# Performance work log

Hardware: AMD Instinct MI355X
Metric: run time of the kernel (lower is better)

## Reference

```python
import jax, jax.numpy as jnp
import numpy as np

N_NODES = 50000
N_EDGES = 800000
IN_F = 128
HID = 32
HEADS = 8
N_CLASSES = 40
OUT_HEADS = 1
NEG_SLOPE = 0.2


def _glorot(key, shape):
    fan_in, fan_out = shape[0], int(np.prod(shape[1:]))
    s = jnp.sqrt(6.0 / (fan_in + fan_out))
    return jax.random.uniform(key, shape, jnp.float32, -s, s)


def setup_inputs() -> dict:
    key = jax.random.key(0)
    ks = jax.random.split(key, 12)
    x = jax.random.normal(ks[0], (N_NODES, IN_F), jnp.float32)
    src = jax.random.randint(ks[1], (N_EDGES,), 0, N_NODES, jnp.int32)
    dst = jax.random.randint(ks[2], (N_EDGES,), 0, N_NODES, jnp.int32)
    # layer 1: IN_F -> HEADS*HID
    W1 = _glorot(ks[3], (IN_F, HEADS * HID))
    al1 = _glorot(ks[4], (HEADS, HID))
    ar1 = _glorot(ks[5], (HEADS, HID))
    # layer 2: HEADS*HID -> HEADS*HID
    W2 = _glorot(ks[6], (HEADS * HID, HEADS * HID))
    al2 = _glorot(ks[7], (HEADS, HID))
    ar2 = _glorot(ks[8], (HEADS, HID))
    # output layer: HEADS*HID -> OUT_HEADS*N_CLASSES (mean over heads)
    Wo = _glorot(ks[9], (HEADS * HID, OUT_HEADS * N_CLASSES))
    alo = _glorot(ks[10], (OUT_HEADS, N_CLASSES))
    aro = _glorot(ks[11], (OUT_HEADS, N_CLASSES))
    return dict(x=x, src=src, dst=dst, W1=W1, al1=al1, ar1=ar1,
                W2=W2, al2=al2, ar2=ar2, Wo=Wo, alo=alo, aro=aro)


def gat_conv(x, src, dst, W, al, ar, concat):
    """Standard GAT layer: per-head projection, edge attention, segment softmax, scatter-sum."""
    N = x.shape[0]
    H, F = al.shape
    h = (x @ W).reshape(N, H, F)                         # [N,H,F]
    el = jnp.einsum('nhf,hf->nh', h, al)                 # [N,H]
    er = jnp.einsum('nhf,hf->nh', h, ar)                 # [N,H]
    e = jax.nn.leaky_relu(el[src] + er[dst], NEG_SLOPE)  # [E,H]
    m = jax.ops.segment_max(e, dst, num_segments=N)      # [N,H] per-dst max
    ex = jnp.exp(e - m[dst])                             # [E,H]
    s = jax.ops.segment_sum(ex, dst, num_segments=N)     # [N,H]
    alpha = ex / (s[dst] + 1e-16)                        # [E,H] softmax over in-edges
    out = jax.ops.segment_sum(h[src] * alpha[:, :, None], dst, num_segments=N)  # [N,H,F]
    return out.reshape(N, H * F) if concat else out.mean(axis=1)


def reference(x, src, dst, W1, al1, ar1, W2, al2, ar2, Wo, alo, aro):
    h = jax.nn.elu(gat_conv(x, src, dst, W1, al1, ar1, concat=True))
    h = jax.nn.elu(gat_conv(h, src, dst, W2, al2, ar2, concat=True))
    out = gat_conv(h, src, dst, Wo, alo, aro, concat=False)  # [N, N_CLASSES]
    return jax.nn.log_softmax(out, axis=1)
```

## Files before the change

kernel.cpp:

```cpp
#include <hip/hip_runtime.h>
#include <hip/hip_bf16.h>

#define N_NODES 50000
#define N_EDGES 800000

typedef __bf16 bf16x8 __attribute__((ext_vector_type(8)));
typedef float f32x4 __attribute__((ext_vector_type(4)));
typedef float f32x2 __attribute__((ext_vector_type(2)));

__device__ __forceinline__ float loadF(const void* p, size_t i, bool isbf) {
    return isbf ? __bfloat162float(((const __hip_bfloat16*)p)[i]) : ((const float*)p)[i];
}
__device__ __forceinline__ float bfbits2f(unsigned short u) {
    return __uint_as_float(((unsigned)u) << 16);
}
__device__ __forceinline__ unsigned short f2bfbits(float f) {
    __hip_bfloat16 h = __float2bfloat16(f);
    return *(unsigned short*)&h;
}
__device__ __forceinline__ unsigned char q_fp8(float v) {
    int p = __builtin_amdgcn_cvt_pk_fp8_f32(v, v, 0, false);
    return (unsigned char)(p & 0xff);
}
__device__ __forceinline__ void acc8_fp8(float ex, uint2 r, float* acc) {
    f32x2 p0 = __builtin_amdgcn_cvt_pk_f32_fp8(r.x, false);
    f32x2 p1 = __builtin_amdgcn_cvt_pk_f32_fp8(r.x, true);
    f32x2 p2 = __builtin_amdgcn_cvt_pk_f32_fp8(r.y, false);
    f32x2 p3 = __builtin_amdgcn_cvt_pk_f32_fp8(r.y, true);
    acc[0] += ex * p0.x; acc[1] += ex * p0.y;
    acc[2] += ex * p1.x; acc[3] += ex * p1.y;
    acc[4] += ex * p2.x; acc[5] += ex * p2.y;
    acc[6] += ex * p3.x; acc[7] += ex * p3.y;
}

__global__ void cvt_hist_k(const void* __restrict__ x, const void* __restrict__ W1,
                           const void* __restrict__ W2, const void* __restrict__ Wo,
                           unsigned short* __restrict__ Xb, unsigned short* __restrict__ W1f,
                           unsigned short* __restrict__ W2f, unsigned short* __restrict__ Wof,
                           int* __restrict__ flag, const int* __restrict__ dst,
                           int* __restrict__ cursor, unsigned short* __restrict__ erank) {
    __shared__ int s_flag;
    int t = threadIdx.x;
    if (t < 64) {
        const unsigned short* xw = (const unsigned short*)x;
        int cnt = 0;
        for (int i = t; i < 512; i += 64) {
            unsigned e = (xw[2 * i] >> 7) & 0xFFu;
            if (e >= 117u && e <= 134u) cnt++;
        }
        for (int off = 32; off; off >>= 1) cnt += __shfl_down(cnt, off, 64);
        if (t == 0) s_flag = (cnt >= 256) ? 1 : 0;
    }
    __syncthreads();
    bool bf = (s_flag != 0);
    int i = blockIdx.x * blockDim.x + t;
    if (i == 0) *flag = s_flag ? 1 : 0;
    if (i < 800000) {
        if (!bf) {
            const float* f = (const float*)x + (size_t)i * 8;
            unsigned short r[8];
            for (int j = 0; j < 8; ++j) r[j] = f2bfbits(f[j]);
            *(uint4*)(Xb + (size_t)i * 8) = *(uint4*)r;
        }
        return;
    }
    int u = i - 800000;
    if (u >= 14336) {
        int e = u - 14336;
        if (e < N_EDGES) {
            int r = atomicAdd(&cursor[dst[e]], 1);
            erank[e] = (unsigned short)r;
        }
        return;
    }
    const void* W; unsigned short* dstp; int Nf, Npad, s, rem;
    if (u < 4096)        { W = W1; dstp = W1f; Nf = 256; Npad = 256; s = u / 1024; rem = u % 1024; }
    else if (u < 12288)  { u -= 4096;  W = W2; dstp = W2f; Nf = 256; Npad = 256; s = u / 1024; rem = u % 1024; }
    else                 { u -= 12288; W = Wo; dstp = Wof; Nf = 40;  Npad = 64;  s = u / 256;  rem = u % 256; }
    int n = rem >> 2, quad = rem & 3;
    unsigned short r[8];
    for (int j = 0; j < 8; ++j) {
        int k = s * 32 + quad * 8 + j;
        r[j] = (n < Nf) ? f2bfbits(loadF(W, (size_t)k * Nf + n, bf)) : (unsigned short)0;
    }
    int uo = (s * Npad + n) * 4 + quad;
    *(uint4*)(dstp + (size_t)uo * 8) = *(uint4*)r;
}

__global__ __launch_bounds__(256)
void scanall_k(const int* __restrict__ deg, int* __restrict__ rowptr, int N, int E) {
    __shared__ int s[256];
    __shared__ int ws[4];
    __shared__ int s_off;
    int t = threadIdx.x, b = blockIdx.x;
    int base = b * 256;
    int acc = 0;
    for (int i = t; i < base; i += 256) acc += deg[i];
    int wave = t >> 6, lane = t & 63;
    for (int off = 32; off; off >>= 1) acc += __shfl_down(acc, off, 64);
    if (lane == 0) ws[wave] = acc;
    __syncthreads();
    if (t == 0) s_off = ws[0] + ws[1] + ws[2] + ws[3];
    __syncthreads();
    int g = base + t;
    int v = (g < N) ? deg[g] : 0;
    s[t] = v; __syncthreads();
    for (int off = 1; off < 256; off <<= 1) {
        int x = (t >= off) ? s[t - off] : 0;
        __syncthreads();
        s[t] += x;
        __syncthreads();
    }
    if (g < N) rowptr[g] = s_off + s[t] - v;
    if (b == 0 && t == 0) rowptr[N] = E;
}

template <int K_, int AMODE>
__device__ __forceinline__
void gemm_attn_body(int bx, int by, int t,
                    const unsigned short* __restrict__ A, const unsigned short* __restrict__ Wf,
                    void* __restrict__ Cout, const void* __restrict__ al,
                    const void* __restrict__ ar, const int* __restrict__ flag,
                    float* __restrict__ el, float* __restrict__ er, int M, int Nfull, int Npad) {
    int row0 = bx * 128, col0 = by * 64;
    int wave = t >> 6, lane = t & 63;
    int wr = (wave >> 1) * 64, wc = (wave & 1) * 32;
    int m16 = lane & 15, quad = lane >> 4;

    const unsigned short* arow[4];
    for (int mt = 0; mt < 4; ++mt) {
        int gr = row0 + wr + mt * 16 + m16;
        int grc = (gr < M) ? gr : (M - 1);
        arow[mt] = A + (size_t)grc * K_ + quad * 8;
    }
    const unsigned short* bbase[2];
    for (int nt = 0; nt < 2; ++nt) {
        int gc = col0 + wc + nt * 16 + m16;
        bbase[nt] = Wf + ((size_t)(gc * 4 + quad) << 3);
    }

    f32x4 acc[4][2] = {};
#pragma unroll
    for (int s = 0; s < K_ / 32; ++s) {
        bf16x8 a[4], b[2];
        for (int mt = 0; mt < 4; ++mt)
            a[mt] = *(const bf16x8*)(arow[mt] + s * 32);
        for (int nt = 0; nt < 2; ++nt)
            b[nt] = *(const bf16x8*)(bbase[nt] + (size_t)s * Npad * 32);
        for (int mt = 0; mt < 4; ++mt)
            for (int nt = 0; nt < 2; ++nt)
                acc[mt][nt] = __builtin_amdgcn_mfma_f32_16x16x32_bf16(
                    a[mt], b[nt], acc[mt][nt], 0, 0, 0);
    }

    if (AMODE == 0) {
        unsigned char* C8 = (unsigned char*)Cout;
        for (int mt = 0; mt < 4; ++mt)
            for (int nt = 0; nt < 2; ++nt)
                for (int r = 0; r < 4; ++r) {
                    int gr = row0 + wr + mt * 16 + quad * 4 + r;
                    int gc = col0 + wc + nt * 16 + m16;
                    if (gr < M)
                        C8[(size_t)gr * 256 + gc] = q_fp8(acc[mt][nt][r]);
                }
    } else {
        __hip_bfloat16* C = (__hip_bfloat16*)Cout;
        for (int mt = 0; mt < 4; ++mt)
            for (int nt = 0; nt < 2; ++nt)
                for (int r = 0; r < 4; ++r) {
                    int gr = row0 + wr + mt * 16 + quad * 4 + r;
                    int gc = col0 + wc + nt * 16 + m16;
                    if (gr < M && gc < Npad)
                        C[(size_t)gr * Npad + gc] = __float2bfloat16(acc[mt][nt][r]);
                }
    }

    bool bf = (*flag != 0);
    float alc[2], arc[2];
    for (int nt = 0; nt < 2; ++nt) {
        int gc = col0 + wc + nt * 16 + m16;
        bool ok = gc < Nfull;
        alc[nt] = ok ? loadF(al, gc, bf) : 0.f;
        arc[nt] = ok ? loadF(ar, gc, bf) : 0.f;
    }
    for (int mt = 0; mt < 4; ++mt)
        for (int r = 0; r < 4; ++r) {
            float pl = acc[mt][0][r] * alc[0] + acc[mt][1][r] * alc[1];
            float pr = acc[mt][0][r] * arc[0] + acc[mt][1][r] * arc[1];
            for (int off = 1; off < 16; off <<= 1) {
                pl += __shfl_xor(pl, off, 64);
                pr += __shfl_xor(pr, off, 64);
            }
            if (m16 == 0) {
                int gr = row0 + wr + mt * 16 + quad * 4 + r;
                if (gr < M) {
                    if (AMODE == 0) {
                        int hd = col0 / 32 + (wave & 1);
                        el[gr * 8 + hd] = pl;
                        er[gr * 8 + hd] = pr;
                    } else {
                        atomicAdd(&el[gr], pl);
                        atomicAdd(&er[gr], pr);
                    }
                }
            }
        }
}

template <int K_, int AMODE>
__global__ __launch_bounds__(256)
void gemm_attn_k(const unsigned short* __restrict__ A, const unsigned short* __restrict__ Wf,
                 void* __restrict__ Cout, const void* __restrict__ al,
                 const void* __restrict__ ar, const int* __restrict__ flag,
                 float* __restrict__ el, float* __restrict__ er, int M, int Nfull, int Npad) {
    gemm_attn_body<K_, AMODE>(blockIdx.x, blockIdx.y, threadIdx.x,
                              A, Wf, Cout, al, ar, flag, el, er, M, Nfull, Npad);
}

__global__ __launch_bounds__(256)
void scatter_gemm1_k(const unsigned short* __restrict__ A, const void* __restrict__ xraw,
                     const unsigned short* __restrict__ Wf,
                     void* __restrict__ Cout, const void* __restrict__ al,
                     const void* __restrict__ ar, const int* __restrict__ flag,
                     float* __restrict__ el, float* __restrict__ er, int M,
                     const int* __restrict__ src, const int* __restrict__ dst,
                     const int* __restrict__ rowptr, const unsigned short* __restrict__ erank,
                     int* __restrict__ ecol, int E, int GB) {
    int b = blockIdx.x, t = threadIdx.x;
    if (b < GB) {
        const unsigned short* Aeff = (*flag != 0) ? (const unsigned short*)xraw : A;
        gemm_attn_body<128, 0>(b >> 2, b & 3, t, Aeff, Wf, Cout, al, ar, flag, el, er, M, 256, 256);
    } else {
        int e = (b - GB) * 256 + t;
        if (e < E) {
            int d = dst[e];
            ecol[rowptr[d] + (int)erank[e]] = src[e];
        }
    }
}

__global__ __launch_bounds__(256)
void aggr1_k(const int* __restrict__ rowptr, const int* __restrict__ ecol,
             const float* __restrict__ el, const float* __restrict__ er,
             const unsigned char* __restrict__ Hp8, __hip_bfloat16* __restrict__ out,
             float* __restrict__ zelo, float* __restrict__ zero_, int N) {
    int t = threadIdx.x;
    int hw = t >> 5, l = t & 31;
    int n = blockIdx.x * 8 + hw;
    if (n >= N) return;
    int beg = rowptr[n], deg = rowptr[n + 1] - beg;

    if (zelo && l == 0) { zelo[n] = 0.f; zero_[n] = 0.f; }

    int hh = l >> 2;
    float er_hh = er[n * 8 + hh];
    float ss = 0.f;
    float acc[8] = {0.f, 0.f, 0.f, 0.f, 0.f, 0.f, 0.f, 0.f};

    int i = 0;
    for (; i + 4 <= deg; i += 4) {
        int s0 = ecol[beg + i], s1 = ecol[beg + i + 1];
        int s2 = ecol[beg + i + 2], s3 = ecol[beg + i + 3];
        uint2 r0 = *(const uint2*)(Hp8 + (size_t)s0 * 256 + l * 8);
        uint2 r1 = *(const uint2*)(Hp8 + (size_t)s1 * 256 + l * 8);
        uint2 r2 = *(const uint2*)(Hp8 + (size_t)s2 * 256 + l * 8);
        uint2 r3 = *(const uint2*)(Hp8 + (size_t)s3 * 256 + l * 8);
        float v0 = el[s0 * 8 + hh] + er_hh;
        float v1 = el[s1 * 8 + hh] + er_hh;
        float v2 = el[s2 * 8 + hh] + er_hh;
        float v3 = el[s3 * 8 + hh] + er_hh;
        v0 = (v0 >= 0.f) ? v0 : 0.2f * v0;
        v1 = (v1 >= 0.f) ? v1 : 0.2f * v1;
        v2 = (v2 >= 0.f) ? v2 : 0.2f * v2;
        v3 = (v3 >= 0.f) ? v3 : 0.2f * v3;
        float e0 = __expf(v0), e1 = __expf(v1), e2 = __expf(v2), e3 = __expf(v3);
        ss += (e0 + e1) + (e2 + e3);
        acc8_fp8(e0, r0, acc);
        acc8_fp8(e1, r1, acc);
        acc8_fp8(e2, r2, acc);
        acc8_fp8(e3, r3, acc);
    }
    for (; i < deg; ++i) {
        int s0 = ecol[beg + i];
        uint2 r0 = *(const uint2*)(Hp8 + (size_t)s0 * 256 + l * 8);
        float v0 = el[s0 * 8 + hh] + er_hh;
        v0 = (v0 >= 0.f) ? v0 : 0.2f * v0;
        float e0 = __expf(v0);
        ss += e0;
        acc8_fp8(e0, r0, acc);
    }

    float inv = 1.f / (ss + 1e-16f);
    unsigned short o[8];
    for (int j = 0; j < 8; ++j) {
        float vv = acc[j] * inv;
        vv = (vv > 0.f) ? vv : expm1f(vv);
        o[j] = f2bfbits(vv);
    }
    *(uint4*)((unsigned short*)out + (size_t)n * 256 + l * 8) = *(uint4*)o;
}

__global__ __launch_bounds__(64)
void aggr_out_k(const int* __restrict__ rowptr, const int* __restrict__ ecol,
                const float* __restrict__ elo, const float* __restrict__ ero,
                const unsigned short* __restrict__ Hp64, void* __restrict__ outp,
                const int* __restrict__ flag, int N) {
    int n = blockIdx.x, l = threadIdx.x;
    int g = l >> 3, f = l & 7;
    int beg = rowptr[n], deg = rowptr[n + 1] - beg;
    float ero_n = ero[n];
    float ss = 0.f;
    float acc[8] = {0.f, 0.f, 0.f, 0.f, 0.f, 0.f, 0.f, 0.f};
    for (int i = g; i < deg; i += 8) {
        int s = ecol[beg + i];
        float v = elo[s] + ero_n;
        v = (v >= 0.f) ? v : 0.2f * v;
        float ex = __expf(v);
        ss += ex;
        uint4 r = *(const uint4*)(Hp64 + (size_t)s * 64 + f * 8);
        unsigned short u[8];
        *(uint4*)u = r;
        for (int j = 0; j < 8; ++j) acc[j] += ex * bfbits2f(u[j]);
    }
    for (int off = 8; off <= 32; off <<= 1) {
        ss += __shfl_xor(ss, off, 64);
        for (int j = 0; j < 8; ++j) acc[j] += __shfl_xor(acc[j], off, 64);
    }
    float inv = 1.f / (ss + 1e-16f);
    float r8[8];
    float vmax = -1e30f;
    for (int j = 0; j < 8; ++j) {
        r8[j] = acc[j] * inv;
        if (f < 5) vmax = fmaxf(vmax, r8[j]);
    }
    for (int off = 1; off <= 4; off <<= 1) vmax = fmaxf(vmax, __shfl_xor(vmax, off, 64));
    float es = 0.f;
    if (f < 5)
        for (int j = 0; j < 8; ++j) es += __expf(r8[j] - vmax);
    for (int off = 1; off <= 4; off <<= 1) es += __shfl_xor(es, off, 64);
    float lse = vmax + logf(es);
    if (f < 5 && g == 0) {
        if (*flag) {
            unsigned short o[8];
            for (int j = 0; j < 8; ++j) o[j] = f2bfbits(r8[j] - lse);
            *(uint4*)((unsigned short*)outp + (size_t)n * 40 + f * 8) = *(uint4*)o;
        } else {
            float* fo = (float*)outp + (size_t)n * 40 + f * 8;
            for (int j = 0; j < 8; ++j) fo[j] = r8[j] - lse;
        }
    }
}

extern "C" void kernel_launch(void* const* d_in, const int* in_sizes, int n_in,
                              void* d_out, int out_size, void* d_ws, size_t ws_size,
                              hipStream_t stream) {
    const int N = N_NODES, E = N_EDGES;
    const void* x   = d_in[0];
    const int* src  = (const int*)d_in[1];
    const int* dst  = (const int*)d_in[2];
    const void* W1  = d_in[3];
    const void* al1 = d_in[4];
    const void* ar1 = d_in[5];
    const void* W2  = d_in[6];
    const void* al2 = d_in[7];
    const void* ar2 = d_in[8];
    const void* Wo  = d_in[9];
    const void* alo = d_in[10];
    const void* aro = d_in[11];

    char* w = (char*)d_ws;
    auto alloc = [&](size_t bytes) { void* p = (void*)w; w += (bytes + 255) & ~(size_t)255; return p; };
    int* flag      = (int*)alloc(4);
    int* rowptr    = (int*)alloc((size_t)(N + 1) * 4);
    int* cursor    = (int*)alloc((size_t)N * 4);
    float* elo     = (float*)alloc((size_t)N * 4);
    float* ero     = (float*)alloc((size_t)N * 4);
    int* ecol      = (int*)alloc((size_t)E * 4);
    unsigned short* erank = (unsigned short*)alloc((size_t)E * 2);
    float* el      = (float*)alloc((size_t)N * 8 * 4);
    float* er      = (float*)alloc((size_t)N * 8 * 4);
    unsigned short* W1f = (unsigned short*)alloc((size_t)128 * 256 * 2);
    unsigned short* W2f = (unsigned short*)alloc((size_t)256 * 256 * 2);
    unsigned short* Wof = (unsigned short*)alloc((size_t)256 * 64 * 2);
    unsigned char* Hp8 = (unsigned char*)alloc((size_t)N * 256);
    __hip_bfloat16* Hagg = (__hip_bfloat16*)alloc((size_t)N * 256 * 2);
    unsigned short* Xb = (unsigned short*)Hagg;
    unsigned short* Hp64 = (unsigned short*)Hp8;

    int NB = (N + 255) / 256;
    int MB = (N + 127) / 128;
    int AB = (N + 7) / 8;
    int GB = MB * 4;
    int SB = (E + 255) / 256;
    int CVT_THREADS = 800000 + 14336 + E;

    hipMemsetAsync(cursor, 0, (size_t)N * 4, stream);
    cvt_hist_k<<<(CVT_THREADS + 255) / 256, 256, 0, stream>>>(
        x, W1, W2, Wo, Xb, W1f, W2f, Wof, flag, dst, cursor, erank);
    scanall_k<<<NB, 256, 0, stream>>>(cursor, rowptr, N, E);
    scatter_gemm1_k<<<GB + SB, 256, 0, stream>>>(
        Xb, x, W1f, Hp8, al1, ar1, flag, el, er, N, src, dst, rowptr, erank, ecol, E, GB);
    aggr1_k<<<AB, 256, 0, stream>>>(rowptr, ecol, el, er, Hp8, Hagg, nullptr, nullptr, N);
    gemm_attn_k<256, 0><<<dim3(MB, 4), 256, 0, stream>>>((const unsigned short*)Hagg, W2f, Hp8, al2, ar2, flag, el, er, N, 256, 256);
    aggr1_k<<<AB, 256, 0, stream>>>(rowptr, ecol, el, er, Hp8, Hagg, elo, ero, N);
    gemm_attn_k<256, 1><<<dim3(MB, 1), 256, 0, stream>>>((const unsigned short*)Hagg, Wof, Hp64, alo, aro, flag, elo, ero, N, 40, 64);
    aggr_out_k<<<N, 64, 0, stream>>>(rowptr, ecol, elo, ero, Hp64, d_out, flag, N);
}
```

Measured before the change: 368.1 us.

## Retile GEMM+attention kernel with full-row blocks, swapped MFMA operands, and prefetch

```diff
diff --git a/kernel.cpp b/kernel.cpp
--- a/kernel.cpp
+++ b/kernel.cpp
@@ -17,10 +17,6 @@
 __device__ __forceinline__ unsigned short f2bfbits(float f) {
     __hip_bfloat16 h = __float2bfloat16(f);
     return *(unsigned short*)&h;
-}
-__device__ __forceinline__ unsigned char q_fp8(float v) {
-    int p = __builtin_amdgcn_cvt_pk_fp8_f32(v, v, 0, false);
-    return (unsigned char)(p & 0xff);
 }
 __device__ __forceinline__ void acc8_fp8(float ex, uint2 r, float* acc) {
     f32x2 p0 = __builtin_amdgcn_cvt_pk_f32_fp8(r.x, false);
@@ -115,109 +111,173 @@
     if (b == 0 && t == 0) rowptr[N] = E;
 }
 
-template <int K_, int AMODE>
+template <int K_, int AMODE, int WROWS, int WCOLS, int NTW>
 __device__ __forceinline__
-void gemm_attn_body(int bx, int by, int t,
+void gemm_attn_body(int bx, int t,
                     const unsigned short* __restrict__ A, const unsigned short* __restrict__ Wf,
                     void* __restrict__ Cout, const void* __restrict__ al,
                     const void* __restrict__ ar, const int* __restrict__ flag,
                     float* __restrict__ el, float* __restrict__ er, int M, int Nfull, int Npad) {
-    int row0 = bx * 128, col0 = by * 64;
+    constexpr int S = K_ / 32;
+    constexpr int RB = WROWS * 32;
     int wave = t >> 6, lane = t & 63;
-    int wr = (wave >> 1) * 64, wc = (wave & 1) * 32;
+    int wrow = wave / WCOLS, wcol = wave % WCOLS;
     int m16 = lane & 15, quad = lane >> 4;
-
-    const unsigned short* arow[4];
-    for (int mt = 0; mt < 4; ++mt) {
-        int gr = row0 + wr + mt * 16 + m16;
+    int rbase = bx * RB + wrow * 32;
+    int cbase = wcol * NTW * 16;
+
+    int aoff[2];
+    for (int mt = 0; mt < 2; ++mt) {
+        int gr = rbase + mt * 16 + m16;
         int grc = (gr < M) ? gr : (M - 1);
-        arow[mt] = A + (size_t)grc * K_ + quad * 8;
-    }
-    const unsigned short* bbase[2];
-    for (int nt = 0; nt < 2; ++nt) {
-        int gc = col0 + wc + nt * 16 + m16;
-        bbase[nt] = Wf + ((size_t)(gc * 4 + quad) << 3);
-    }
-
-    f32x4 acc[4][2] = {};
-#pragma unroll
-    for (int s = 0; s < K_ / 32; ++s) {
-        bf16x8 a[4], b[2];
-        for (int mt = 0; mt < 4; ++mt)
-            a[mt] = *(const bf16x8*)(arow[mt] + s * 32);
-        for (int nt = 0; nt < 2; ++nt)
-            b[nt] = *(const bf16x8*)(bbase[nt] + (size_t)s * Npad * 32);
-        for (int mt = 0; mt < 4; ++mt)
-            for (int nt = 0; nt < 2; ++nt)
+        aoff[mt] = grc * K_ + quad * 8;
+    }
+    int boff[NTW];
+    for (int nt = 0; nt < NTW; ++nt) {
+        int gc = cbase + nt * 16 + m16;
+        boff[nt] = (gc * 4 + quad) * 8;
+    }
+    int bstep = Npad * 32;
+
+    f32x4 acc[2][NTW] = {};
+    bf16x8 a0[2], a1[2], b0[NTW], b1[NTW];
+#pragma unroll
+    for (int mt = 0; mt < 2; ++mt) a0[mt] = *(const bf16x8*)(A + aoff[mt]);
+#pragma unroll
+    for (int nt = 0; nt < NTW; ++nt) b0[nt] = *(const bf16x8*)(Wf + boff[nt]);
+#pragma unroll
+    for (int s = 0; s < S; ++s) {
+        if (s + 1 < S) {
+#pragma unroll
+            for (int mt = 0; mt < 2; ++mt)
+                a1[mt] = *(const bf16x8*)(A + aoff[mt] + (s + 1) * 32);
+#pragma unroll
+            for (int nt = 0; nt < NTW; ++nt)
+                b1[nt] = *(const bf16x8*)(Wf + boff[nt] + (size_t)(s + 1) * bstep);
+        }
+#pragma unroll
+        for (int mt = 0; mt < 2; ++mt)
+#pragma unroll
+            for (int nt = 0; nt < NTW; ++nt)
                 acc[mt][nt] = __builtin_amdgcn_mfma_f32_16x16x32_bf16(
-                    a[mt], b[nt], acc[mt][nt], 0, 0, 0);
+                    b0[nt], a0[mt], acc[mt][nt], 0, 0, 0);
+        if (s + 1 < S) {
+#pragma unroll
+            for (int mt = 0; mt < 2; ++mt) a0[mt] = a1[mt];
+#pragma unroll
+            for (int nt = 0; nt < NTW; ++nt) b0[nt] = b1[nt];
+        }
     }
 
     if (AMODE == 0) {
         unsigned char* C8 = (unsigned char*)Cout;
-        for (int mt = 0; mt < 4; ++mt)
-            for (int nt = 0; nt < 2; ++nt)
-                for (int r = 0; r < 4; ++r) {
-                    int gr = row0 + wr + mt * 16 + quad * 4 + r;
-                    int gc = col0 + wc + nt * 16 + m16;
-                    if (gr < M)
-                        C8[(size_t)gr * 256 + gc] = q_fp8(acc[mt][nt][r]);
+#pragma unroll
+        for (int mt = 0; mt < 2; ++mt) {
+            int gr = rbase + mt * 16 + m16;
+            if (gr < M) {
+#pragma unroll
+                for (int nt = 0; nt < NTW; ++nt) {
+                    int u = __builtin_amdgcn_cvt_pk_fp8_f32(acc[mt][nt][0], acc[mt][nt][1], 0, false);
+                    u = __builtin_amdgcn_cvt_pk_fp8_f32(acc[mt][nt][2], acc[mt][nt][3], u, true);
+                    *(int*)(C8 + (size_t)gr * 256 + cbase + nt * 16 + quad * 4) = u;
                 }
+            }
+        }
     } else {
         __hip_bfloat16* C = (__hip_bfloat16*)Cout;
-        for (int mt = 0; mt < 4; ++mt)
-            for (int nt = 0; nt < 2; ++nt)
-                for (int r = 0; r < 4; ++r) {
-                    int gr = row0 + wr + mt * 16 + quad * 4 + r;
-                    int gc = col0 + wc + nt * 16 + m16;
-                    if (gr < M && gc < Npad)
-                        C[(size_t)gr * Npad + gc] = __float2bfloat16(acc[mt][nt][r]);
-                }
-    }
-
-    bool bf = (*flag != 0);
-    float alc[2], arc[2];
-    for (int nt = 0; nt < 2; ++nt) {
-        int gc = col0 + wc + nt * 16 + m16;
-        bool ok = gc < Nfull;
-        alc[nt] = ok ? loadF(al, gc, bf) : 0.f;
-        arc[nt] = ok ? loadF(ar, gc, bf) : 0.f;
-    }
-    for (int mt = 0; mt < 4; ++mt)
-        for (int r = 0; r < 4; ++r) {
-            float pl = acc[mt][0][r] * alc[0] + acc[mt][1][r] * alc[1];
-            float pr = acc[mt][0][r] * arc[0] + acc[mt][1][r] * arc[1];
-            for (int off = 1; off < 16; off <<= 1) {
-                pl += __shfl_xor(pl, off, 64);
-                pr += __shfl_xor(pr, off, 64);
-            }
-            if (m16 == 0) {
-                int gr = row0 + wr + mt * 16 + quad * 4 + r;
-                if (gr < M) {
-                    if (AMODE == 0) {
-                        int hd = col0 / 32 + (wave & 1);
-                        el[gr * 8 + hd] = pl;
-                        er[gr * 8 + hd] = pr;
-                    } else {
-                        atomicAdd(&el[gr], pl);
-                        atomicAdd(&er[gr], pr);
-                    }
+#pragma unroll
+        for (int mt = 0; mt < 2; ++mt) {
+            int gr = rbase + mt * 16 + m16;
+            if (gr < M) {
+#pragma unroll
+                for (int nt = 0; nt < NTW; ++nt) {
+                    ushort4 o;
+                    o.x = f2bfbits(acc[mt][nt][0]);
+                    o.y = f2bfbits(acc[mt][nt][1]);
+                    o.z = f2bfbits(acc[mt][nt][2]);
+                    o.w = f2bfbits(acc[mt][nt][3]);
+                    *(ushort4*)((unsigned short*)C + (size_t)gr * Npad + cbase + nt * 16 + quad * 4) = o;
                 }
             }
         }
-}
-
-template <int K_, int AMODE>
-__global__ __launch_bounds__(256)
+    }
+
+    bool bf = (*flag != 0);
+    if (AMODE == 0) {
+#pragma unroll
+        for (int h = 0; h < NTW / 2; ++h) {
+            float alc2[2][4], arc2[2][4];
+#pragma unroll
+            for (int j = 0; j < 2; ++j)
+#pragma unroll
+                for (int r = 0; r < 4; ++r) {
+                    int gc = cbase + (2 * h + j) * 16 + quad * 4 + r;
+                    bool ok = gc < Nfull;
+                    alc2[j][r] = ok ? loadF(al, gc, bf) : 0.f;
+                    arc2[j][r] = ok ? loadF(ar, gc, bf) : 0.f;
+                }
+#pragma unroll
+            for (int mt = 0; mt < 2; ++mt) {
+                float pl = 0.f, pr = 0.f;
+#pragma unroll
+                for (int j = 0; j < 2; ++j)
+#pragma unroll
+                    for (int r = 0; r < 4; ++r) {
+                        pl += acc[mt][2 * h + j][r] * alc2[j][r];
+                        pr += acc[mt][2 * h + j][r] * arc2[j][r];
+                    }
+                pl += __shfl_xor(pl, 16, 64); pl += __shfl_xor(pl, 32, 64);
+                pr += __shfl_xor(pr, 16, 64); pr += __shfl_xor(pr, 32, 64);
+                int gr = rbase + mt * 16 + m16;
+                if (quad == 0 && gr < M) {
+                    int habs = wcol * (NTW / 2) + h;
+                    el[gr * 8 + habs] = pl;
+                    er[gr * 8 + habs] = pr;
+                }
+            }
+        }
+    } else {
+        float pl[2] = {0.f, 0.f}, pr[2] = {0.f, 0.f};
+#pragma unroll
+        for (int nt = 0; nt < NTW; ++nt) {
+            float alc4[4], arc4[4];
+#pragma unroll
+            for (int r = 0; r < 4; ++r) {
+                int gc = cbase + nt * 16 + quad * 4 + r;
+                bool ok = gc < Nfull;
+                alc4[r] = ok ? loadF(al, gc, bf) : 0.f;
+                arc4[r] = ok ? loadF(ar, gc, bf) : 0.f;
+            }
+#pragma unroll
+            for (int mt = 0; mt < 2; ++mt)
+#pragma unroll
+                for (int r = 0; r < 4; ++r) {
+                    pl[mt] += acc[mt][nt][r] * alc4[r];
+                    pr[mt] += acc[mt][nt][r] * arc4[r];
+                }
+        }
+#pragma unroll
+        for (int mt = 0; mt < 2; ++mt) {
+            float l = pl[mt], r = pr[mt];
+            l += __shfl_xor(l, 16, 64); l += __shfl_xor(l, 32, 64);
+            r += __shfl_xor(r, 16, 64); r += __shfl_xor(r, 32, 64);
+            int gr = rbase + mt * 16 + m16;
+            if (quad == 0 && gr < M) { el[gr] = l; er[gr] = r; }
+        }
+    }
+}
+
+template <int K_, int AMODE, int WROWS, int WCOLS, int NTW>
+__global__ __launch_bounds__(256, 2)
 void gemm_attn_k(const unsigned short* __restrict__ A, const unsigned short* __restrict__ Wf,
                  void* __restrict__ Cout, const void* __restrict__ al,
                  const void* __restrict__ ar, const int* __restrict__ flag,
                  float* __restrict__ el, float* __restrict__ er, int M, int Nfull, int Npad) {
-    gemm_attn_body<K_, AMODE>(blockIdx.x, blockIdx.y, threadIdx.x,
-                              A, Wf, Cout, al, ar, flag, el, er, M, Nfull, Npad);
-}
-
-__global__ __launch_bounds__(256)
+    gemm_attn_body<K_, AMODE, WROWS, WCOLS, NTW>(blockIdx.x, threadIdx.x,
+                                                 A, Wf, Cout, al, ar, flag, el, er, M, Nfull, Npad);
+}
+
+__global__ __launch_bounds__(256, 2)
 void scatter_gemm1_k(const unsigned short* __restrict__ A, const void* __restrict__ xraw,
                      const unsigned short* __restrict__ Wf,
                      void* __restrict__ Cout, const void* __restrict__ al,
@@ -229,7 +289,7 @@
     int b = blockIdx.x, t = threadIdx.x;
     if (b < GB) {
         const unsigned short* Aeff = (*flag != 0) ? (const unsigned short*)xraw : A;
-        gemm_attn_body<128, 0>(b >> 2, b & 3, t, Aeff, Wf, Cout, al, ar, flag, el, er, M, 256, 256);
+        gemm_attn_body<128, 0, 2, 2, 8>(b, t, Aeff, Wf, Cout, al, ar, flag, el, er, M, 256, 256);
     } else {
         int e = (b - GB) * 256 + t;
         if (e < E) {
@@ -242,15 +302,12 @@
 __global__ __launch_bounds__(256)
 void aggr1_k(const int* __restrict__ rowptr, const int* __restrict__ ecol,
              const float* __restrict__ el, const float* __restrict__ er,
-             const unsigned char* __restrict__ Hp8, __hip_bfloat16* __restrict__ out,
-             float* __restrict__ zelo, float* __restrict__ zero_, int N) {
+             const unsigned char* __restrict__ Hp8, __hip_bfloat16* __restrict__ out, int N) {
     int t = threadIdx.x;
     int hw = t >> 5, l = t & 31;
     int n = blockIdx.x * 8 + hw;
     if (n >= N) return;
     int beg = rowptr[n], deg = rowptr[n + 1] - beg;
-
-    if (zelo && l == 0) { zelo[n] = 0.f; zero_[n] = 0.f; }
 
     int hh = l >> 2;
     float er_hh = er[n * 8 + hh];
@@ -388,9 +445,9 @@
     unsigned short* Hp64 = (unsigned short*)Hp8;
 
     int NB = (N + 255) / 256;
-    int MB = (N + 127) / 128;
+    int GB = (N + 63) / 64;
+    int OB = (N + 127) / 128;
     int AB = (N + 7) / 8;
-    int GB = MB * 4;
     int SB = (E + 255) / 256;
     int CVT_THREADS = 800000 + 14336 + E;
 
@@ -400,9 +457,11 @@
     scanall_k<<<NB, 256, 0, stream>>>(cursor, rowptr, N, E);
     scatter_gemm1_k<<<GB + SB, 256, 0, stream>>>(
         Xb, x, W1f, Hp8, al1, ar1, flag, el, er, N, src, dst, rowptr, erank, ecol, E, GB);
-    aggr1_k<<<AB, 256, 0, stream>>>(rowptr, ecol, el, er, Hp8, Hagg, nullptr, nullptr, N);
-    gemm_attn_k<256, 0><<<dim3(MB, 4), 256, 0, stream>>>((const unsigned short*)Hagg, W2f, Hp8, al2, ar2, flag, el, er, N, 256, 256);
-    aggr1_k<<<AB, 256, 0, stream>>>(rowptr, ecol, el, er, Hp8, Hagg, elo, ero, N);
-    gemm_attn_k<256, 1><<<dim3(MB, 1), 256, 0, stream>>>((const unsigned short*)Hagg, Wof, Hp64, alo, aro, flag, elo, ero, N, 40, 64);
+    aggr1_k<<<AB, 256, 0, stream>>>(rowptr, ecol, el, er, Hp8, Hagg, N);
+    gemm_attn_k<256, 0, 2, 2, 8><<<GB, 256, 0, stream>>>(
+        (const unsigned short*)Hagg, W2f, Hp8, al2, ar2, flag, el, er, N, 256, 256);
+    aggr1_k<<<AB, 256, 0, stream>>>(rowptr, ecol, el, er, Hp8, Hagg, N);
+    gemm_attn_k<256, 1, 4, 1, 4><<<OB, 256, 0, stream>>>(
+        (const unsigned short*)Hagg, Wof, Hp64, alo, aro, flag, elo, ero, N, 40, 64);
     aggr_out_k<<<N, 64, 0, stream>>>(rowptr, ecol, elo, ero, Hp64, d_out, flag, N);
 }
```

Result: faster. 354.3 us (-3.8%).
